# Optimization experiments

Measured on AMD Instinct MI355X. Metric: run time of the kernel, lower is better.

The kernel has to match this reference:

```python
import jax, jax.numpy as jnp
import numpy as np

N = 768                       # atoms
E = N * (N - 1)               # complete directed graph edges
DIM = 64                      # hidden dim
CUT = 5.0                     # rbf high
NC = 50                       # n_centers = ceil(5/0.1)
ODIM = 1                      # output_dim
NCONV = 3
_centers_np = np.linspace(0.0, CUT, NC)
CENTERS = jnp.asarray(_centers_np, jnp.float32)
GAP = float(_centers_np[1] - _centers_np[0])
RO_IN = 2 * ODIM + NC         # readout input: 2*output_dim + rbf fan_out = 52


def softplus_bt(x, beta, thr):
    # torch.nn.Softplus(beta, threshold): linear above threshold
    bx = beta * x
    return jnp.where(bx > thr, x, jax.nn.softplus(bx) / beta)


def rbf(d):
    # exp(-(1/gap) * (d - mu_k)^2); d: (..., 1) -> (..., NC)
    return jnp.exp((-1.0 / GAP) * (d - CENTERS) ** 2)


def setup_inputs() -> dict:
    key = jax.random.key(0)
    ks = jax.random.split(key, 24)
    atom_types = jax.random.randint(ks[0], (N,), 0, 100)
    edge_distances = jax.random.uniform(ks[1], (E, 1), jnp.float32) * CUT
    # complete directed graph, edge order matches the nested i,j loop (i!=j)
    ii = np.repeat(np.arange(N), N)
    jj = np.tile(np.arange(N), N)
    m = ii != jj
    src = jnp.asarray(ii[m], jnp.int32)
    dst = jnp.asarray(jj[m], jnp.int32)

    def p(k, shape, fan):
        return jax.random.normal(k, shape, jnp.float32) / np.sqrt(fan)

    embedding = p(ks[2], (100, DIM), DIM).at[0].set(0.0)  # padding_idx=0
    L = NCONV
    return {
        'atom_types': atom_types, 'edge_distances': edge_distances,
        'src': src, 'dst': dst, 'embedding': embedding,
        'w1': p(ks[3], (L, DIM, DIM), DIM),                 # node_layer1 (no bias)
        'pw1': p(ks[4], (L, NC, DIM), NC), 'pb1': p(ks[5], (L, DIM), NC),
        'pw2': p(ks[6], (L, DIM, DIM), DIM), 'pb2': p(ks[7], (L, DIM), DIM),
        'qw1': p(ks[8], (L, DIM, DIM), DIM), 'qb1': p(ks[9], (L, DIM), DIM),
        'qw2': p(ks[10], (L, DIM, DIM), DIM), 'qb2': p(ks[11], (L, DIM), DIM),
        'au_w1': p(ks[12], (DIM, 64), DIM), 'au_b1': p(ks[13], (64,), DIM),
        'au_w2': p(ks[14], (64, ODIM), 64), 'au_b2': p(ks[15], (ODIM,), 64),
        'ro_w1': p(ks[16], (RO_IN, 64), RO_IN), 'ro_b1': p(ks[17], (64,), RO_IN),
        'ro_w2': p(ks[18], (64, 2), 64), 'ro_b2': p(ks[19], (2,), 64),
    }


def reference(atom_types, edge_distances, src, dst, embedding,
              w1, pw1, pb1, pw2, pb2, qw1, qb1, qw2, qb2,
              au_w1, au_b1, au_w2, au_b2, ro_w1, ro_b1, ro_w2, ro_b2):
    h = embedding[atom_types]                       # (N, DIM)
    rbf_out = rbf(edge_distances)                   # (E, NC)
    for l in range(NCONV):
        nw = h @ w1[l]                              # node weights (N, DIM)
        e = softplus_bt(rbf_out @ pw1[l] + pb1[l], 0.5, 14) @ pw2[l] + pb2[l]  # (E, DIM)
        msg = nw[src] * e                           # gather-mul (E, DIM)
        agg = jax.ops.segment_sum(msg, dst, num_segments=N)  # scatter-sum (N, DIM)
        upd = softplus_bt(agg @ qw1[l] + qb1[l], 0.5, 14) @ qw2[l] + qb2[l]
        h = h + upd
    # atom_update with ShiftSoftplus (beta=1, shift=2, threshold=20)
    ha = softplus_bt(h @ au_w1 + au_b1, 1.0, 20) - jnp.log(jnp.float32(2.0))
    ha = ha @ au_w2 + au_b2                         # (N, ODIM)
    # readout over all ordered pairs i!=j, in edge order == (src, dst)
    edge_feat = jnp.concatenate([ha[src], ha[dst], rbf_out], axis=-1)  # (E, 52)
    logits = jax.nn.relu(edge_feat @ ro_w1 + ro_b1) @ ro_w2 + ro_b2    # (E, 2)
    return jax.nn.softmax(logits, axis=-1)
```

## Files before the change

### kernel.cpp

```cpp
#include <hip/hip_runtime.h>
#include <hip/hip_fp16.h>

#define NATOMS 768
#define NM1    767
#define NEDGE  (768*767)
#define DIM    64
#define NC     50
#define GAPF   (5.0f/49.0f)
#define NIGAP  (-49.0f/5.0f)
#define G      512
#define STEPF  (5.0f/511.0f)
#define INVSTEP (511.0f/5.0f)
#define LN2F   0.693147180559945f

#define WS_H     0
#define WS_NWA   49152
#define WS_NWB   73728
#define WS_HA    98304
#define WS_DISTT 99328
#define WS_TT    689152

__device__ __forceinline__ float softplus05(float x) {
    float bx = 0.5f * x;
    return (bx > 14.0f) ? x : 2.0f * __logf(1.0f + __expf(bx));
}
__device__ __forceinline__ int lane_bcast_i(int v, int l) {
    return __builtin_amdgcn_readlane(v, l);
}
__device__ __forceinline__ float lane_bcast_f(float v, int l) {
    return __uint_as_float((unsigned)__builtin_amdgcn_readlane((int)__float_as_uint(v), l));
}

__global__ __launch_bounds__(256)
void k_pre(const int* __restrict__ types, const float* __restrict__ dist,
           const float* __restrict__ emb, const float* __restrict__ w1all,
           const float* __restrict__ pw1, const float* __restrict__ pb1,
           const float* __restrict__ pw2, const float* __restrict__ pb2,
           const float* __restrict__ row1, const float* __restrict__ rob1,
           float* __restrict__ ws) {
    __shared__ float s_t[4 * 64];
    __shared__ float s_tile[64][65];
    const int tid = threadIdx.x, widx = tid >> 6, c = tid & 63;
    float*  h     = ws + WS_H;
    __half* nwh   = (__half*)(ws + WS_NWA);
    float*  distT = ws + WS_DISTT;
    __half* TTh   = (__half*)(ws + WS_TT);
    const int b = blockIdx.x;

    if (b < 512) {
        const int w = b * 4 + widx, tbl = w >> 9, g = w & 511;
        const float d = g * STEPF;
        float val;
        if (tbl < 3) {
            const float* W1 = pw1 + tbl * NC * DIM;
            float t1 = pb1[tbl * DIM + c];
            for (int k = 0; k < NC; ++k) {
                float x = d - GAPF * (float)k;
                t1 = fmaf(__expf(NIGAP * x * x), W1[k * DIM + c], t1);
            }
            s_t[widx * 64 + c] = softplus05(t1);
            const float* W2 = pw2 + tbl * DIM * DIM;
            val = pb2[tbl * DIM + c];
            #pragma unroll 8
            for (int k = 0; k < DIM; ++k)
                val = fmaf(s_t[widx * 64 + k], W2[k * DIM + c], val);
        } else {
            val = rob1[c];
            for (int k = 0; k < NC; ++k) {
                float x = d - GAPF * (float)k;
                val = fmaf(__expf(NIGAP * x * x), row1[(2 + k) * DIM + c], val);
            }
        }
        __half* TTt = TTh + tbl * (G * DIM * 2);
        TTt[(g * DIM + c) * 2] = __float2half(val);
        if (g > 0) TTt[((g - 1) * DIM + c) * 2 + 1] = __float2half(val);
    } else if (b < 704) {
        const int i = (b - 512) * 4 + widx;
        float hv = emb[types[i] * DIM + c];
        h[i * DIM + c] = hv;
        s_t[widx * 64 + c] = hv;
        float acc = 0.0f;
        #pragma unroll 8
        for (int k = 0; k < DIM; ++k)
            acc = fmaf(s_t[widx * 64 + k], w1all[k * DIM + c], acc);
        nwh[(i >> 1) * 128 + c * 2 + (i & 1)] = __float2half(acc);
    } else {
        const int t = b - 704;
        const int I0 = (t / 12) * 64, J0 = (t % 12) * 64;
        #pragma unroll 4
        for (int r = 0; r < 16; ++r) {
            const int i = I0 + widx * 16 + r;
            const int j = J0 + c;
            s_tile[widx * 16 + r][c] =
                (i == j) ? 0.0f : dist[i * NM1 + (j - (j > i))];
        }
        __syncthreads();
        #pragma unroll 4
        for (int r = 0; r < 16; ++r) {
            const int j = J0 + widx * 16 + r;
            const int i = I0 + c;
            distT[j * NATOMS + i] = s_tile[c][widx * 16 + r];
        }
    }
}

__global__ __launch_bounds__(512)
void k_edgeupd(const __half2* __restrict__ TTl, const float* __restrict__ distT,
               const __half2* __restrict__ nwin,
               const float* __restrict__ qw1, const float* __restrict__ qb1,
               const float* __restrict__ qw2, const float* __restrict__ qb2,
               float* __restrict__ h,
               const float* __restrict__ wnext, __half* __restrict__ nwout,
               const float* __restrict__ auw1, const float* __restrict__ aub1,
               const float* __restrict__ auw2, const float* __restrict__ aub2,
               float* __restrict__ ha, int last) {
    __shared__ float s_part[8][64];
    __shared__ float s_upd[192];
    const int tid = threadIdx.x, widx = tid >> 6, c = tid & 63;
    const int j = blockIdx.x;
    const int s0 = widx * 96;

    const char* TTb = (const char*)TTl + c * 4;
    float csum = 0.0f;
    {
        float d = distT[j * NATOMS + s0 + c];
        float pos = d * INVSTEP;
        int g = (int)pos;
        g = (g < 0) ? 0 : ((g > 510) ? 510 : g);
        float f = pos - (float)g;
        int kx = g * 256;
        const __half2* nwrow = nwin + (s0 >> 1) * 64 + c;
        #pragma unroll 8
        for (int t = 0; t < 32; ++t) {
            int kx0 = lane_bcast_i(kx, 2 * t);
            int kx1 = lane_bcast_i(kx, 2 * t + 1);
            float f0 = lane_bcast_f(f, 2 * t);
            float f1 = lane_bcast_f(f, 2 * t + 1);
            float2 ta = __half22float2(*(const __half2*)(TTb + kx0));
            float2 tb = __half22float2(*(const __half2*)(TTb + kx1));
            float2 nwf = __half22float2(nwrow[t * 64]);
            float e0 = fmaf(f0, ta.y - ta.x, ta.x);
            float e1 = fmaf(f1, tb.y - tb.x, tb.x);
            csum = fmaf(e0, nwf.x, csum);
            csum = fmaf(e1, nwf.y, csum);
        }
    }
    {
        float d = distT[j * NATOMS + s0 + 64 + (c & 31)];
        float pos = d * INVSTEP;
        int g = (int)pos;
        g = (g < 0) ? 0 : ((g > 510) ? 510 : g);
        float f = pos - (float)g;
        int kx = g * 256;
        const __half2* nwrow = nwin + ((s0 + 64) >> 1) * 64 + c;
        #pragma unroll 8
        for (int t = 0; t < 16; ++t) {
            int kx0 = lane_bcast_i(kx, 2 * t);
            int kx1 = lane_bcast_i(kx, 2 * t + 1);
            float f0 = lane_bcast_f(f, 2 * t);
            float f1 = lane_bcast_f(f, 2 * t + 1);
            float2 ta = __half22float2(*(const __half2*)(TTb + kx0));
            float2 tb = __half22float2(*(const __half2*)(TTb + kx1));
            float2 nwf = __half22float2(nwrow[t * 64]);
            float e0 = fmaf(f0, ta.y - ta.x, ta.x);
            float e1 = fmaf(f1, tb.y - tb.x, tb.x);
            csum = fmaf(e0, nwf.x, csum);
            csum = fmaf(e1, nwf.y, csum);
        }
    }
    s_part[widx][c] = csum;
    __syncthreads();

    if (widx == 0) {
        float tot = 0.0f;
        #pragma unroll
        for (int w8 = 0; w8 < 8; ++w8) tot += s_part[w8][c];
        float2 t0 = __half22float2(*(const __half2*)TTb);
        float nwj = __half2float(((const __half*)nwin)[(j >> 1) * 128 + c * 2 + (j & 1)]);
        tot -= t0.x * nwj;
        s_upd[c] = tot;
        float t = qb1[c];
        #pragma unroll 8
        for (int k = 0; k < DIM; ++k) t = fmaf(s_upd[k], qw1[k * DIM + c], t);
        s_upd[64 + c] = softplus05(t);
        float o = qb2[c];
        #pragma unroll 8
        for (int k = 0; k < DIM; ++k) o = fmaf(s_upd[64 + k], qw2[k * DIM + c], o);
        float hn = h[j * DIM + c] + o;
        h[j * DIM + c] = hn;
        s_upd[128 + c] = hn;
        if (!last) {
            float v = 0.0f;
            #pragma unroll 8
            for (int k = 0; k < DIM; ++k) v = fmaf(s_upd[128 + k], wnext[k * DIM + c], v);
            nwout[(j >> 1) * 128 + c * 2 + (j & 1)] = __float2half(v);
        } else {
            float t2 = aub1[c];
            #pragma unroll 8
            for (int k = 0; k < DIM; ++k) t2 = fmaf(s_upd[128 + k], auw1[k * DIM + c], t2);
            t2 = ((t2 > 20.0f) ? t2 : __logf(1.0f + __expf(t2))) - LN2F;
            float v = t2 * auw2[c];
            #pragma unroll
            for (int s = 32; s > 0; s >>= 1) v += __shfl_down(v, s, 64);
            if (c == 0) ha[j] = v + aub2[0];
        }
    }
}

__global__ __launch_bounds__(256)
void k_ro(const float* __restrict__ dist, const int* __restrict__ src,
          const int* __restrict__ dst, const float* __restrict__ ha,
          const __half2* __restrict__ TTro,
          const float* __restrict__ row1, const float* __restrict__ row2,
          const float* __restrict__ rob2, float* __restrict__ out) {
    __shared__ float s_h[4][16 * 65];
    __shared__ float s_w2[128];
    const int tid = threadIdx.x, widx = tid >> 6, c = tid & 63;
    if (tid < 128) s_w2[tid] = row2[tid];
    __syncthreads();
    const int ebase = (blockIdx.x * 4 + widx) * 64;

    int kxv; float ff, fa, fb;
    {
        int eg = ebase + c;
        float d = dist[eg];
        float pos = d * INVSTEP;
        int kk = (int)pos;
        kk = (kk < 0) ? 0 : ((kk > 510) ? 510 : kk);
        kxv = kk * 256;
        ff = pos - (float)kk;
        fa = ha[src[eg]];
        fb = ha[dst[eg]];
    }
    const char* TTb2 = (const char*)TTro + c * 4;
    const float wa = row1[c], wb = row1[DIM + c];
    const int e2 = (c >> 1) & 15, p2 = c & 1, kh = c >> 5;
    const float bias2 = (kh == 0) ? rob2[p2] : 0.0f;
    float* sh = s_h[widx];
    #pragma unroll
    for (int ch = 0; ch < 4; ++ch) {
        #pragma unroll 8
        for (int e = 0; e < 16; ++e) {
            const int le = ch * 16 + e;
            int kxu   = lane_bcast_i(kxv, le);
            float fu  = lane_bcast_f(ff, le);
            float fau = lane_bcast_f(fa, le);
            float fbu = lane_bcast_f(fb, le);
            float2 tt = __half22float2(*(const __half2*)(TTb2 + kxu));
            float hv = fmaf(fu, tt.y - tt.x, tt.x);
            hv = fmaf(fau, wa, hv);
            hv = fmaf(fbu, wb, hv);
            sh[e * 65 + c] = fmaxf(hv, 0.0f);
        }
        float lsum = bias2;
        #pragma unroll 8
        for (int k8 = 0; k8 < 32; ++k8) {
            int k = kh * 32 + k8;
            lsum = fmaf(sh[e2 * 65 + k], s_w2[2 * k + p2], lsum);
        }
        lsum += __shfl_xor(lsum, 32, 64);
        float other = __shfl_xor(lsum, 1, 64);
        float m = fmaxf(lsum, other);
        float ea = __expf(lsum - m), eb = __expf(other - m);
        float r = ea / (ea + eb);
        if (c < 32) out[ebase * 2 + ch * 32 + c] = r;
    }
}

extern "C" void kernel_launch(void* const* d_in, const int* in_sizes, int n_in,
                              void* d_out, int out_size, void* d_ws, size_t ws_size,
                              hipStream_t stream) {
    const int*   types = (const int*)d_in[0];
    const float* dist  = (const float*)d_in[1];
    const int*   srcI  = (const int*)d_in[2];
    const int*   dstI  = (const int*)d_in[3];
    const float* emb   = (const float*)d_in[4];
    const float* w1    = (const float*)d_in[5];
    const float* pw1   = (const float*)d_in[6];
    const float* pb1   = (const float*)d_in[7];
    const float* pw2   = (const float*)d_in[8];
    const float* pb2   = (const float*)d_in[9];
    const float* qw1   = (const float*)d_in[10];
    const float* qb1   = (const float*)d_in[11];
    const float* qw2   = (const float*)d_in[12];
    const float* qb2   = (const float*)d_in[13];
    const float* auw1  = (const float*)d_in[14];
    const float* aub1  = (const float*)d_in[15];
    const float* auw2  = (const float*)d_in[16];
    const float* aub2  = (const float*)d_in[17];
    const float* row1  = (const float*)d_in[18];
    const float* rob1  = (const float*)d_in[19];
    const float* row2  = (const float*)d_in[20];
    const float* rob2  = (const float*)d_in[21];

    float* ws   = (float*)d_ws;
    float* outp = (float*)d_out;
    const __half2* TT = (const __half2*)(ws + WS_TT);
    __half2* nwbuf[2] = { (__half2*)(ws + WS_NWA), (__half2*)(ws + WS_NWB) };

    k_pre<<<848, 256, 0, stream>>>(types, dist, emb, w1, pw1, pb1, pw2, pb2,
                                   row1, rob1, ws);
    for (int l = 0; l < 3; ++l) {
        k_edgeupd<<<768, 512, 0, stream>>>(TT + l * (G * DIM),
            ws + WS_DISTT, nwbuf[l & 1],
            qw1 + l * DIM * DIM, qb1 + l * DIM,
            qw2 + l * DIM * DIM, qb2 + l * DIM,
            ws + WS_H,
            (l < 2) ? (w1 + (l + 1) * DIM * DIM) : w1, (__half*)nwbuf[(l + 1) & 1],
            auw1, aub1, auw2, aub2, ws + WS_HA, (l == 2) ? 1 : 0);
    }
    k_ro<<<2301, 256, 0, stream>>>(dist, srcI, dstI, ws + WS_HA, TT + 3 * (G * DIM),
                                   row1, row2, rob2, outp);
}
```

Measured before the change: 185.5 us.

## Fuse all stages into one persistent kernel with software grid barriers

Replaces the five separate launches (precompute, three edge-update layers, readout) with a single persistent kernel of 256 blocks × 1024 threads that synchronises stages through an atomic-counter grid barrier in workspace, reset by a memset before launch. Each block now handles three destination atoms per layer and strides over readout edge groups. The distance transpose drops its shared-memory tile and writes directly with divided indices. The aim is to remove kernel launch gaps and tail effects. In exchange it relies on all 256 blocks being co-resident, otherwise the barrier deadlocks, and the smaller grid may reduce parallelism and occupancy in the readout phase.

```diff
diff --git a/kernel.cpp b/kernel.cpp
--- a/kernel.cpp
+++ b/kernel.cpp
@@ -19,6 +19,10 @@
 #define WS_HA    98304
 #define WS_DISTT 99328
 #define WS_TT    689152
+#define WS_BAR   820224
+
+#define NBLK 256
+#define NTHR 1024
 
 __device__ __forceinline__ float softplus05(float x) {
     float bx = 0.5f * x;
@@ -31,239 +35,238 @@
     return __uint_as_float((unsigned)__builtin_amdgcn_readlane((int)__float_as_uint(v), l));
 }
 
-__global__ __launch_bounds__(256)
-void k_pre(const int* __restrict__ types, const float* __restrict__ dist,
-           const float* __restrict__ emb, const float* __restrict__ w1all,
-           const float* __restrict__ pw1, const float* __restrict__ pb1,
-           const float* __restrict__ pw2, const float* __restrict__ pb2,
-           const float* __restrict__ row1, const float* __restrict__ rob1,
-           float* __restrict__ ws) {
-    __shared__ float s_t[4 * 64];
-    __shared__ float s_tile[64][65];
+__device__ __forceinline__ void gbar(int* cnt, int* gen) {
+    __syncthreads();
+    if (threadIdx.x == 0) {
+        __threadfence();
+        int g = __hip_atomic_load(gen, __ATOMIC_RELAXED, __HIP_MEMORY_SCOPE_AGENT);
+        int a = __hip_atomic_fetch_add(cnt, 1, __ATOMIC_ACQ_REL, __HIP_MEMORY_SCOPE_AGENT);
+        if (a == NBLK - 1) {
+            __hip_atomic_store(cnt, 0, __ATOMIC_RELAXED, __HIP_MEMORY_SCOPE_AGENT);
+            __hip_atomic_fetch_add(gen, 1, __ATOMIC_ACQ_REL, __HIP_MEMORY_SCOPE_AGENT);
+        } else {
+            while (__hip_atomic_load(gen, __ATOMIC_ACQUIRE, __HIP_MEMORY_SCOPE_AGENT) == g)
+                __builtin_amdgcn_s_sleep(2);
+        }
+        __threadfence();
+    }
+    __syncthreads();
+}
+
+__global__ __launch_bounds__(NTHR)
+void k_fused(const int* __restrict__ types, const float* __restrict__ dist,
+             const int* __restrict__ srcI, const int* __restrict__ dstI,
+             const float* __restrict__ emb, const float* __restrict__ w1,
+             const float* __restrict__ pw1, const float* __restrict__ pb1,
+             const float* __restrict__ pw2, const float* __restrict__ pb2,
+             const float* __restrict__ qw1, const float* __restrict__ qb1,
+             const float* __restrict__ qw2, const float* __restrict__ qb2,
+             const float* __restrict__ auw1, const float* __restrict__ aub1,
+             const float* __restrict__ auw2, const float* __restrict__ aub2,
+             const float* __restrict__ row1, const float* __restrict__ rob1,
+             const float* __restrict__ row2, const float* __restrict__ rob2,
+             float* __restrict__ ws, float* __restrict__ out) {
+    __shared__ float s_t[16][64];
+    __shared__ float s_part[3][16][64];
+    __shared__ float s_upd[3][192];
+    __shared__ float s_h[16][16 * 65];
+    __shared__ float s_w2[128];
+
     const int tid = threadIdx.x, widx = tid >> 6, c = tid & 63;
-    float*  h     = ws + WS_H;
-    __half* nwh   = (__half*)(ws + WS_NWA);
-    float*  distT = ws + WS_DISTT;
-    __half* TTh   = (__half*)(ws + WS_TT);
-    const int b = blockIdx.x;
-
-    if (b < 512) {
-        const int w = b * 4 + widx, tbl = w >> 9, g = w & 511;
-        const float d = g * STEPF;
-        float val;
-        if (tbl < 3) {
-            const float* W1 = pw1 + tbl * NC * DIM;
-            float t1 = pb1[tbl * DIM + c];
-            for (int k = 0; k < NC; ++k) {
-                float x = d - GAPF * (float)k;
-                t1 = fmaf(__expf(NIGAP * x * x), W1[k * DIM + c], t1);
-            }
-            s_t[widx * 64 + c] = softplus05(t1);
-            const float* W2 = pw2 + tbl * DIM * DIM;
-            val = pb2[tbl * DIM + c];
+    const int blk = blockIdx.x;
+    int* cnt = (int*)(ws + WS_BAR);
+    int* gen = cnt + 1;
+
+    float*   h     = ws + WS_H;
+    float*   haV   = ws + WS_HA;
+    float*   distT = ws + WS_DISTT;
+    __half*  TTh   = (__half*)(ws + WS_TT);
+    const __half2* TT = (const __half2*)(ws + WS_TT);
+    __half2* nwb[2] = { (__half2*)(ws + WS_NWA), (__half2*)(ws + WS_NWB) };
+
+    {
+        const int W = blk * 16 + widx;
+        if (W < 2048) {
+            const int tbl = W >> 9, g = W & 511;
+            const float d = g * STEPF;
+            float val;
+            if (tbl < 3) {
+                const float* W1 = pw1 + tbl * NC * DIM;
+                float t1 = pb1[tbl * DIM + c];
+                for (int k = 0; k < NC; ++k) {
+                    float x = d - GAPF * (float)k;
+                    t1 = fmaf(__expf(NIGAP * x * x), W1[k * DIM + c], t1);
+                }
+                s_t[widx][c] = softplus05(t1);
+                const float* W2 = pw2 + tbl * DIM * DIM;
+                val = pb2[tbl * DIM + c];
+                #pragma unroll 8
+                for (int k = 0; k < DIM; ++k)
+                    val = fmaf(s_t[widx][k], W2[k * DIM + c], val);
+            } else {
+                val = rob1[c];
+                for (int k = 0; k < NC; ++k) {
+                    float x = d - GAPF * (float)k;
+                    val = fmaf(__expf(NIGAP * x * x), row1[(2 + k) * DIM + c], val);
+                }
+            }
+            __half* TTt = TTh + tbl * (G * DIM * 2);
+            TTt[(g * DIM + c) * 2] = __float2half(val);
+            if (g > 0) TTt[((g - 1) * DIM + c) * 2 + 1] = __float2half(val);
+        } else if (W < 2816) {
+            const int i = W - 2048;
+            float hv = emb[types[i] * DIM + c];
+            h[i * DIM + c] = hv;
+            s_t[widx][c] = hv;
+            float acc = 0.0f;
             #pragma unroll 8
             for (int k = 0; k < DIM; ++k)
-                val = fmaf(s_t[widx * 64 + k], W2[k * DIM + c], val);
-        } else {
-            val = rob1[c];
-            for (int k = 0; k < NC; ++k) {
-                float x = d - GAPF * (float)k;
-                val = fmaf(__expf(NIGAP * x * x), row1[(2 + k) * DIM + c], val);
-            }
-        }
-        __half* TTt = TTh + tbl * (G * DIM * 2);
-        TTt[(g * DIM + c) * 2] = __float2half(val);
-        if (g > 0) TTt[((g - 1) * DIM + c) * 2 + 1] = __float2half(val);
-    } else if (b < 704) {
-        const int i = (b - 512) * 4 + widx;
-        float hv = emb[types[i] * DIM + c];
-        h[i * DIM + c] = hv;
-        s_t[widx * 64 + c] = hv;
-        float acc = 0.0f;
-        #pragma unroll 8
-        for (int k = 0; k < DIM; ++k)
-            acc = fmaf(s_t[widx * 64 + k], w1all[k * DIM + c], acc);
-        nwh[(i >> 1) * 128 + c * 2 + (i & 1)] = __float2half(acc);
-    } else {
-        const int t = b - 704;
-        const int I0 = (t / 12) * 64, J0 = (t % 12) * 64;
-        #pragma unroll 4
-        for (int r = 0; r < 16; ++r) {
-            const int i = I0 + widx * 16 + r;
-            const int j = J0 + c;
-            s_tile[widx * 16 + r][c] =
-                (i == j) ? 0.0f : dist[i * NM1 + (j - (j > i))];
+                acc = fmaf(s_t[widx][k], w1[k * DIM + c], acc);
+            ((__half*)nwb[0])[(i >> 1) * 128 + c * 2 + (i & 1)] = __float2half(acc);
+        } else if (W < 3392) {
+            const int u = W - 2816;
+            for (int t = 0; t < 16; ++t) {
+                const int idx = u * 1024 + t * 64 + c;
+                const int jj = idx / NATOMS, ii = idx - jj * NATOMS;
+                distT[idx] = (ii == jj) ? 0.0f : dist[ii * NM1 + (jj - (jj > ii))];
+            }
+        }
+    }
+    gbar(cnt, gen);
+
+    for (int l = 0; l < 3; ++l) {
+        const __half2* TTl   = TT + l * (G * DIM);
+        const __half2* nwin  = nwb[l & 1];
+        __half*        nwout = (__half*)nwb[(l + 1) & 1];
+        const float* qw1l = qw1 + l * DIM * DIM; const float* qb1l = qb1 + l * DIM;
+        const float* qw2l = qw2 + l * DIM * DIM; const float* qb2l = qb2 + l * DIM;
+        const float* wnx  = (l < 2) ? (w1 + (l + 1) * DIM * DIM) : w1;
+        const int last = (l == 2);
+
+        const char* TTb = (const char*)TTl + c * 4;
+        for (int dd = 0; dd < 3; ++dd) {
+            const int j = blk * 3 + dd;
+            const int s0 = widx * 48;
+            float d = distT[j * NATOMS + s0 + (c < 48 ? c : 47)];
+            float pos = d * INVSTEP;
+            int g = (int)pos;
+            g = (g < 0) ? 0 : ((g > 510) ? 510 : g);
+            float f = pos - (float)g;
+            int kx = g * 256;
+            const __half2* nwrow = nwin + (s0 >> 1) * 64 + c;
+            float csum = 0.0f;
+            #pragma unroll 8
+            for (int t = 0; t < 24; ++t) {
+                int kx0 = lane_bcast_i(kx, 2 * t);
+                int kx1 = lane_bcast_i(kx, 2 * t + 1);
+                float f0 = lane_bcast_f(f, 2 * t);
+                float f1 = lane_bcast_f(f, 2 * t + 1);
+                float2 ta = __half22float2(*(const __half2*)(TTb + kx0));
+                float2 tb = __half22float2(*(const __half2*)(TTb + kx1));
+                float2 nwf = __half22float2(nwrow[t * 64]);
+                float e0 = fmaf(f0, ta.y - ta.x, ta.x);
+                float e1 = fmaf(f1, tb.y - tb.x, tb.x);
+                csum = fmaf(e0, nwf.x, csum);
+                csum = fmaf(e1, nwf.y, csum);
+            }
+            s_part[dd][widx][c] = csum;
         }
         __syncthreads();
-        #pragma unroll 4
-        for (int r = 0; r < 16; ++r) {
-            const int j = J0 + widx * 16 + r;
-            const int i = I0 + c;
-            distT[j * NATOMS + i] = s_tile[c][widx * 16 + r];
-        }
+
+        if (widx < 3) {
+            const int dd = widx;
+            const int j = blk * 3 + dd;
+            float tot = 0.0f;
+            #pragma unroll
+            for (int w16 = 0; w16 < 16; ++w16) tot += s_part[dd][w16][c];
+            float2 t0 = __half22float2(*(const __half2*)TTb);
+            float nwj = __half2float(((const __half*)nwin)[(j >> 1) * 128 + c * 2 + (j & 1)]);
+            tot -= t0.x * nwj;
+            float* su = s_upd[dd];
+            su[c] = tot;
+            float t = qb1l[c];
+            #pragma unroll 8
+            for (int k = 0; k < DIM; ++k) t = fmaf(su[k], qw1l[k * DIM + c], t);
+            su[64 + c] = softplus05(t);
+            float o = qb2l[c];
+            #pragma unroll 8
+            for (int k = 0; k < DIM; ++k) o = fmaf(su[64 + k], qw2l[k * DIM + c], o);
+            float hn = h[j * DIM + c] + o;
+            h[j * DIM + c] = hn;
+            su[128 + c] = hn;
+            if (!last) {
+                float v = 0.0f;
+                #pragma unroll 8
+                for (int k = 0; k < DIM; ++k) v = fmaf(su[128 + k], wnx[k * DIM + c], v);
+                nwout[(j >> 1) * 128 + c * 2 + (j & 1)] = __float2half(v);
+            } else {
+                float t2 = aub1[c];
+                #pragma unroll 8
+                for (int k = 0; k < DIM; ++k) t2 = fmaf(su[128 + k], auw1[k * DIM + c], t2);
+                t2 = ((t2 > 20.0f) ? t2 : __logf(1.0f + __expf(t2))) - LN2F;
+                float v = t2 * auw2[c];
+                #pragma unroll
+                for (int s = 32; s > 0; s >>= 1) v += __shfl_down(v, s, 64);
+                if (c == 0) haV[j] = v + aub2[0];
+            }
+        }
+        gbar(cnt, gen);
     }
-}
-
-__global__ __launch_bounds__(512)
-void k_edgeupd(const __half2* __restrict__ TTl, const float* __restrict__ distT,
-               const __half2* __restrict__ nwin,
-               const float* __restrict__ qw1, const float* __restrict__ qb1,
-               const float* __restrict__ qw2, const float* __restrict__ qb2,
-               float* __restrict__ h,
-               const float* __restrict__ wnext, __half* __restrict__ nwout,
-               const float* __restrict__ auw1, const float* __restrict__ aub1,
-               const float* __restrict__ auw2, const float* __restrict__ aub2,
-               float* __restrict__ ha, int last) {
-    __shared__ float s_part[8][64];
-    __shared__ float s_upd[192];
-    const int tid = threadIdx.x, widx = tid >> 6, c = tid & 63;
-    const int j = blockIdx.x;
-    const int s0 = widx * 96;
-
-    const char* TTb = (const char*)TTl + c * 4;
-    float csum = 0.0f;
-    {
-        float d = distT[j * NATOMS + s0 + c];
-        float pos = d * INVSTEP;
-        int g = (int)pos;
-        g = (g < 0) ? 0 : ((g > 510) ? 510 : g);
-        float f = pos - (float)g;
-        int kx = g * 256;
-        const __half2* nwrow = nwin + (s0 >> 1) * 64 + c;
-        #pragma unroll 8
-        for (int t = 0; t < 32; ++t) {
-            int kx0 = lane_bcast_i(kx, 2 * t);
-            int kx1 = lane_bcast_i(kx, 2 * t + 1);
-            float f0 = lane_bcast_f(f, 2 * t);
-            float f1 = lane_bcast_f(f, 2 * t + 1);
-            float2 ta = __half22float2(*(const __half2*)(TTb + kx0));
-            float2 tb = __half22float2(*(const __half2*)(TTb + kx1));
-            float2 nwf = __half22float2(nwrow[t * 64]);
-            float e0 = fmaf(f0, ta.y - ta.x, ta.x);
-            float e1 = fmaf(f1, tb.y - tb.x, tb.x);
-            csum = fmaf(e0, nwf.x, csum);
-            csum = fmaf(e1, nwf.y, csum);
-        }
-    }
-    {
-        float d = distT[j * NATOMS + s0 + 64 + (c & 31)];
-        float pos = d * INVSTEP;
-        int g = (int)pos;
-        g = (g < 0) ? 0 : ((g > 510) ? 510 : g);
-        float f = pos - (float)g;
-        int kx = g * 256;
-        const __half2* nwrow = nwin + ((s0 + 64) >> 1) * 64 + c;
-        #pragma unroll 8
-        for (int t = 0; t < 16; ++t) {
-            int kx0 = lane_bcast_i(kx, 2 * t);
-            int kx1 = lane_bcast_i(kx, 2 * t + 1);
-            float f0 = lane_bcast_f(f, 2 * t);
-            float f1 = lane_bcast_f(f, 2 * t + 1);
-            float2 ta = __half22float2(*(const __half2*)(TTb + kx0));
-            float2 tb = __half22float2(*(const __half2*)(TTb + kx1));
-            float2 nwf = __half22float2(nwrow[t * 64]);
-            float e0 = fmaf(f0, ta.y - ta.x, ta.x);
-            float e1 = fmaf(f1, tb.y - tb.x, tb.x);
-            csum = fmaf(e0, nwf.x, csum);
-            csum = fmaf(e1, nwf.y, csum);
-        }
-    }
-    s_part[widx][c] = csum;
-    __syncthreads();
-
-    if (widx == 0) {
-        float tot = 0.0f;
-        #pragma unroll
-        for (int w8 = 0; w8 < 8; ++w8) tot += s_part[w8][c];
-        float2 t0 = __half22float2(*(const __half2*)TTb);
-        float nwj = __half2float(((const __half*)nwin)[(j >> 1) * 128 + c * 2 + (j & 1)]);
-        tot -= t0.x * nwj;
-        s_upd[c] = tot;
-        float t = qb1[c];
-        #pragma unroll 8
-        for (int k = 0; k < DIM; ++k) t = fmaf(s_upd[k], qw1[k * DIM + c], t);
-        s_upd[64 + c] = softplus05(t);
-        float o = qb2[c];
-        #pragma unroll 8
-        for (int k = 0; k < DIM; ++k) o = fmaf(s_upd[64 + k], qw2[k * DIM + c], o);
-        float hn = h[j * DIM + c] + o;
-        h[j * DIM + c] = hn;
-        s_upd[128 + c] = hn;
-        if (!last) {
-            float v = 0.0f;
-            #pragma unroll 8
-            for (int k = 0; k < DIM; ++k) v = fmaf(s_upd[128 + k], wnext[k * DIM + c], v);
-            nwout[(j >> 1) * 128 + c * 2 + (j & 1)] = __float2half(v);
-        } else {
-            float t2 = aub1[c];
-            #pragma unroll 8
-            for (int k = 0; k < DIM; ++k) t2 = fmaf(s_upd[128 + k], auw1[k * DIM + c], t2);
-            t2 = ((t2 > 20.0f) ? t2 : __logf(1.0f + __expf(t2))) - LN2F;
-            float v = t2 * auw2[c];
-            #pragma unroll
-            for (int s = 32; s > 0; s >>= 1) v += __shfl_down(v, s, 64);
-            if (c == 0) ha[j] = v + aub2[0];
-        }
-    }
-}
-
-__global__ __launch_bounds__(256)
-void k_ro(const float* __restrict__ dist, const int* __restrict__ src,
-          const int* __restrict__ dst, const float* __restrict__ ha,
-          const __half2* __restrict__ TTro,
-          const float* __restrict__ row1, const float* __restrict__ row2,
-          const float* __restrict__ rob2, float* __restrict__ out) {
-    __shared__ float s_h[4][16 * 65];
-    __shared__ float s_w2[128];
-    const int tid = threadIdx.x, widx = tid >> 6, c = tid & 63;
+
     if (tid < 128) s_w2[tid] = row2[tid];
     __syncthreads();
-    const int ebase = (blockIdx.x * 4 + widx) * 64;
-
-    int kxv; float ff, fa, fb;
     {
-        int eg = ebase + c;
-        float d = dist[eg];
-        float pos = d * INVSTEP;
-        int kk = (int)pos;
-        kk = (kk < 0) ? 0 : ((kk > 510) ? 510 : kk);
-        kxv = kk * 256;
-        ff = pos - (float)kk;
-        fa = ha[src[eg]];
-        fb = ha[dst[eg]];
-    }
-    const char* TTb2 = (const char*)TTro + c * 4;
-    const float wa = row1[c], wb = row1[DIM + c];
-    const int e2 = (c >> 1) & 15, p2 = c & 1, kh = c >> 5;
-    const float bias2 = (kh == 0) ? rob2[p2] : 0.0f;
-    float* sh = s_h[widx];
-    #pragma unroll
-    for (int ch = 0; ch < 4; ++ch) {
-        #pragma unroll 8
-        for (int e = 0; e < 16; ++e) {
-            const int le = ch * 16 + e;
-            int kxu   = lane_bcast_i(kxv, le);
-            float fu  = lane_bcast_f(ff, le);
-            float fau = lane_bcast_f(fa, le);
-            float fbu = lane_bcast_f(fb, le);
-            float2 tt = __half22float2(*(const __half2*)(TTb2 + kxu));
-            float hv = fmaf(fu, tt.y - tt.x, tt.x);
-            hv = fmaf(fau, wa, hv);
-            hv = fmaf(fbu, wb, hv);
-            sh[e * 65 + c] = fmaxf(hv, 0.0f);
-        }
-        float lsum = bias2;
-        #pragma unroll 8
-        for (int k8 = 0; k8 < 32; ++k8) {
-            int k = kh * 32 + k8;
-            lsum = fmaf(sh[e2 * 65 + k], s_w2[2 * k + p2], lsum);
-        }
-        lsum += __shfl_xor(lsum, 32, 64);
-        float other = __shfl_xor(lsum, 1, 64);
-        float m = fmaxf(lsum, other);
-        float ea = __expf(lsum - m), eb = __expf(other - m);
-        float r = ea / (ea + eb);
-        if (c < 32) out[ebase * 2 + ch * 32 + c] = r;
+        const __half2* TTro = TT + 3 * (G * DIM);
+        const char* TTb2 = (const char*)TTro + c * 4;
+        const float wa = row1[c], wb = row1[DIM + c];
+        const int e2 = (c >> 1) & 15, p2 = c & 1, kh = c >> 5;
+        const float bias2 = (kh == 0) ? rob2[p2] : 0.0f;
+        float* sh = s_h[widx];
+        for (int t16 = 0; t16 < 3; ++t16) {
+            const int gidx = blk * 16 + widx + t16 * 4096;
+            if (gidx >= NEDGE / 64) continue;
+            const int ebase = gidx * 64;
+            int kxv; float ff, fa, fb;
+            {
+                int eg = ebase + c;
+                float d = dist[eg];
+                float pos = d * INVSTEP;
+                int kk = (int)pos;
+                kk = (kk < 0) ? 0 : ((kk > 510) ? 510 : kk);
+                kxv = kk * 256;
+                ff = pos - (float)kk;
+                fa = haV[srcI[eg]];
+                fb = haV[dstI[eg]];
+            }
+            #pragma unroll
+            for (int ch = 0; ch < 4; ++ch) {
+                #pragma unroll 8
+                for (int e = 0; e < 16; ++e) {
+                    const int le = ch * 16 + e;
+                    int kxu   = lane_bcast_i(kxv, le);
+                    float fu  = lane_bcast_f(ff, le);
+                    float fau = lane_bcast_f(fa, le);
+                    float fbu = lane_bcast_f(fb, le);
+                    float2 tt = __half22float2(*(const __half2*)(TTb2 + kxu));
+                    float hv = fmaf(fu, tt.y - tt.x, tt.x);
+                    hv = fmaf(fau, wa, hv);
+                    hv = fmaf(fbu, wb, hv);
+                    sh[e * 65 + c] = fmaxf(hv, 0.0f);
+                }
+                float lsum = bias2;
+                #pragma unroll 8
+                for (int k8 = 0; k8 < 32; ++k8) {
+                    int k = kh * 32 + k8;
+                    lsum = fmaf(sh[e2 * 65 + k], s_w2[2 * k + p2], lsum);
+                }
+                lsum += __shfl_xor(lsum, 32, 64);
+                float other = __shfl_xor(lsum, 1, 64);
+                float m = fmaxf(lsum, other);
+                float ea = __expf(lsum - m), eb = __expf(other - m);
+                float r = ea / (ea + eb);
+                if (c < 32) out[ebase * 2 + ch * 32 + c] = r;
+            }
+        }
     }
 }
 
@@ -295,20 +298,10 @@
 
     float* ws   = (float*)d_ws;
     float* outp = (float*)d_out;
-    const __half2* TT = (const __half2*)(ws + WS_TT);
-    __half2* nwbuf[2] = { (__half2*)(ws + WS_NWA), (__half2*)(ws + WS_NWB) };
-
-    k_pre<<<848, 256, 0, stream>>>(types, dist, emb, w1, pw1, pb1, pw2, pb2,
-                                   row1, rob1, ws);
-    for (int l = 0; l < 3; ++l) {
-        k_edgeupd<<<768, 512, 0, stream>>>(TT + l * (G * DIM),
-            ws + WS_DISTT, nwbuf[l & 1],
-            qw1 + l * DIM * DIM, qb1 + l * DIM,
-            qw2 + l * DIM * DIM, qb2 + l * DIM,
-            ws + WS_H,
-            (l < 2) ? (w1 + (l + 1) * DIM * DIM) : w1, (__half*)nwbuf[(l + 1) & 1],
-            auw1, aub1, auw2, aub2, ws + WS_HA, (l == 2) ? 1 : 0);
-    }
-    k_ro<<<2301, 256, 0, stream>>>(dist, srcI, dstI, ws + WS_HA, TT + 3 * (G * DIM),
-                                   row1, row2, rob2, outp);
-}
+
+    hipMemsetAsync(ws + WS_BAR, 0, 2 * sizeof(int), stream);
+    k_fused<<<NBLK, NTHR, 0, stream>>>(types, dist, srcI, dstI, emb, w1,
+                                       pw1, pb1, pw2, pb2, qw1, qb1, qw2, qb2,
+                                       auw1, aub1, auw2, aub2,
+                                       row1, rob1, row2, rob2, ws, outp);
+}
```

After: 403.7 us. 2.18x slower.
